# Kernel tuning notes

Hardware: AMD Instinct MI355X
Metric: run time of the kernel (lower is better)

## Reference

```python
import jax, jax.numpy as jnp
import numpy as np

EMBED_DIM = 1024
NUM_HEADS = 16
HEAD_DIM = EMBED_DIM // NUM_HEADS


def setup_inputs() -> dict:
    key = jax.random.key(0)
    kx, kw1, kb1, kw2, kb2 = jax.random.split(key, 5)
    D = EMBED_DIM
    # torch nn.Linear default init: U(-1/sqrt(in), 1/sqrt(in)); use scaled uniform
    lim = 1.0 / np.sqrt(D)
    return {
        "x": jax.random.normal(kx, (2, 2048, D), dtype=jnp.float32),
        "w_qkv": jax.random.uniform(kw1, (D, 3 * D), jnp.float32, -lim, lim),
        "b_qkv": jax.random.uniform(kb1, (3 * D,), jnp.float32, -lim, lim),
        "w_o": jax.random.uniform(kw2, (D, D), jnp.float32, -lim, lim),
        "b_o": jax.random.uniform(kb2, (D,), jnp.float32, -lim, lim),
    }


def reference(x, w_qkv, b_qkv, w_o, b_o):
    B, S, D = x.shape
    H, hd = NUM_HEADS, HEAD_DIM
    qkv = x @ w_qkv + b_qkv                       # [B,S,3D]
    qkv = qkv.reshape(B, S, H, 3, hd)             # per-head [q|k|v] blocks of size hd
    q = qkv[:, :, :, 0].transpose(0, 2, 1, 3)     # [B,H,S,hd]
    k = qkv[:, :, :, 1].transpose(0, 2, 1, 3)
    v = qkv[:, :, :, 2].transpose(0, 2, 1, 3)
    scale = hd ** -0.5
    scores = jnp.einsum('bhqd,bhkd->bhqk', q, k) * scale
    attn = jax.nn.softmax(scores, axis=-1)
    out = jnp.einsum('bhqk,bhkd->bhqd', attn, v)  # [B,H,S,hd]
    out = out.transpose(0, 2, 1, 3).reshape(B, S, D)
    return out @ w_o + b_o
```

## Files before the change

kernel.cpp:

```cpp
#include <hip/hip_runtime.h>

typedef __attribute__((ext_vector_type(8))) _Float16 half8;
typedef __attribute__((ext_vector_type(4))) _Float16 half4;
typedef __attribute__((ext_vector_type(4))) float f32x4;
typedef __attribute__((ext_vector_type(16))) float f32x16;
typedef __attribute__((ext_vector_type(4))) int i32x4;

typedef __attribute__((address_space(1))) void* gptr_t;
typedef __attribute__((address_space(3))) void* lptr_t;
#define GLL16(g, l) __builtin_amdgcn_global_load_lds((gptr_t)(g), (lptr_t)(l), 16, 0, 0)

__device__ __forceinline__ float fast_exp2(float x) {
  float r;
  asm volatile("v_exp_f32 %0, %1" : "=v"(r) : "v"(x));
  return r;
}


__global__ void cvt_x_kernel(const float* __restrict__ x, _Float16* __restrict__ xh) {
  size_t i = (size_t)blockIdx.x * blockDim.x + threadIdx.x;
  float4 v = *reinterpret_cast<const float4*>(x + i * 4);
  half4 o = { (_Float16)v.x, (_Float16)v.y, (_Float16)v.z, (_Float16)v.w };
  *reinterpret_cast<half4*>(xh + i * 4) = o;
}

__global__ void transpose_cvt_kernel(const float* __restrict__ w, _Float16* __restrict__ wt, int N) {
  int tid = blockIdx.x * blockDim.x + threadIdx.x;
  int n = tid % N, kc = tid / N;
  half8 o;
#pragma unroll
  for (int i = 0; i < 8; ++i) o[i] = (_Float16)w[(size_t)(kc * 8 + i) * N + n];
  *reinterpret_cast<half8*>(wt + (size_t)n * 1024 + kc * 8) = o;
}


template<int EPI>
__global__ __launch_bounds__(256, 2)
void gemm16(const _Float16* __restrict__ A, const _Float16* __restrict__ Bt,
            const float* __restrict__ bias,
            _Float16* __restrict__ qh, _Float16* __restrict__ kh,
            _Float16* __restrict__ vT, float* __restrict__ outf) {
  __shared__ __align__(16) _Float16 Ah[128 * 64];
  __shared__ __align__(16) _Float16 Bh[128 * 64];
  const int t = threadIdx.x;
  const int w = t >> 6, ln = t & 63, G = ln >> 4, c = ln & 15;
  const int m0 = blockIdx.y * 128, n0 = blockIdx.x * 128;
  const int wr = w >> 1, wc = w & 1;
  f32x4 acc[4][4] = {};
  for (int kt = 0; kt < 1024; kt += 64) {
#pragma unroll
    for (int i = 0; i < 4; ++i) {
      int ch = i * 256 + t;
      int row = ch >> 3, kc = ch & 7;
      int kk = kt + ((kc ^ (row & 7)) << 3);
      int ldsbase = (i * 256 + w * 64) * 8;
      GLL16(A + (size_t)(m0 + row) * 1024 + kk, Ah + ldsbase);
      GLL16(Bt + (size_t)(n0 + row) * 1024 + kk, Bh + ldsbase);
    }
    __syncthreads();
    half8 aF[2][4], bF[2][4];
#pragma unroll
    for (int ks = 0; ks < 2; ++ks)
#pragma unroll
      for (int i = 0; i < 4; ++i) {
        int ra = wr * 64 + i * 16 + c;
        aF[ks][i] = *reinterpret_cast<const half8*>(&Ah[ra * 64 + (((ks * 4 + G) ^ (ra & 7)) << 3)]);
        int rb = wc * 64 + i * 16 + c;
        bF[ks][i] = *reinterpret_cast<const half8*>(&Bh[rb * 64 + (((ks * 4 + G) ^ (rb & 7)) << 3)]);
      }
#pragma unroll
    for (int ks = 0; ks < 2; ++ks)
#pragma unroll
      for (int mi = 0; mi < 4; ++mi)
#pragma unroll
        for (int ni = 0; ni < 4; ++ni)
          acc[mi][ni] = __builtin_amdgcn_mfma_f32_16x16x32_f16(aF[ks][mi], bF[ks][ni], acc[mi][ni], 0, 0, 0);
    __syncthreads();
  }
  const int mbase = m0 + wr * 64, nbase = n0 + wc * 64;
  const int Gp = ((G & 1) << 1) | (G >> 1);
#pragma unroll
  for (int ni = 0; ni < 4; ++ni) {
    int n = nbase + ni * 16 + c;
    float bv = bias[n];
    if (EPI == 0) {
      int h = n / 192;
      int rem = n - h * 192;
      int tt = rem >> 6, d = rem & 63;
#pragma unroll
      for (int mi = 0; mi < 4; ++mi) {
        if (tt == 2) {
          int mb = mbase + mi * 16;
          int bb = mb >> 11, s0 = mb & 2047;
          size_t bh = (size_t)(bb * 16 + h);
          half4 o = { (_Float16)(acc[mi][ni][0] + bv), (_Float16)(acc[mi][ni][1] + bv),
                      (_Float16)(acc[mi][ni][2] + bv), (_Float16)(acc[mi][ni][3] + bv) };
          *reinterpret_cast<half4*>(&vT[(bh * 64 + d) * 2048 + s0 + 4 * Gp]) = o;
        } else {
#pragma unroll
          for (int r = 0; r < 4; ++r) {
            int m = mbase + mi * 16 + 4 * G + r;
            int bb = m >> 11, s = m & 2047;
            float val = acc[mi][ni][r] + bv;
            size_t bh = (size_t)(bb * 16 + h);
            if (tt == 0) qh[(bh * 2048 + s) * 64 + d] = (_Float16)(val * (0.125f * 1.44269504089f));
            else         kh[(bh * 2048 + s) * 64 + d] = (_Float16)val;
          }
        }
      }
    } else {
#pragma unroll
      for (int mi = 0; mi < 4; ++mi)
#pragma unroll
        for (int r = 0; r < 4; ++r) {
          int m = mbase + mi * 16 + 4 * G + r;
          outf[(size_t)m * 1024 + n] = acc[mi][ni][r] + bv;
        }
    }
  }
}


__global__ __launch_bounds__(256, 2)
void attn_kernel(const _Float16* __restrict__ qh, const _Float16* __restrict__ kh,
                 const _Float16* __restrict__ vT, _Float16* __restrict__ ao) {
  __shared__ __align__(16) _Float16 Kt[2][64 * 64];
  __shared__ __align__(16) _Float16 Vt[2][64 * 64];
  const int t = threadIdx.x;
  const int w = t >> 6, ln = t & 63, lo = ln & 31, hi = ln >> 5;
  const int bid = blockIdx.x;
  const int xcd = bid & 7, tt = bid >> 3;
  const int bh = xcd * 4 + (tt >> 4);
  const int qb = tt & 15;
  const int q0 = qb * 128 + w * 32;
  const _Float16* qp = qh + (size_t)bh * 2048 * 64;
  const _Float16* kp = kh + (size_t)bh * 2048 * 64;
  const _Float16* vp = vT + (size_t)bh * 64 * 2048;

  half8 qf[4];
#pragma unroll
  for (int sl = 0; sl < 4; ++sl)
    qf[sl] = *reinterpret_cast<const half8*>(qp + (size_t)(q0 + lo) * 64 + sl * 16 + hi * 8);

  f32x16 O0 = {}, O1 = {};
  float mrun = -INFINITY, lsum = 0.f;

  auto stage = [&](int b, int jt) {
#pragma unroll
    for (int i = 0; i < 2; ++i) {
      int ch = i * 256 + t;
      int row = ch >> 3, cc = ch & 7;
      int sw = ((cc ^ (row & 7)) << 3);
      int ldsbase = (i * 256 + w * 64) * 8;
      GLL16(kp + (size_t)(jt + row) * 64 + sw, &Kt[b][ldsbase]);
      GLL16(vp + (size_t)row * 2048 + jt + sw, &Vt[b][ldsbase]);
    }
  };

  stage(0, 0);
  __syncthreads();

  for (int it = 0; it < 32; ++it) {
    const int buf = it & 1;
    if (it < 31) stage(buf ^ 1, (it + 1) * 64);

    f32x16 st0 = {}, st1 = {};
    __builtin_amdgcn_s_setprio(1);
#pragma unroll
    for (int sl = 0; sl < 4; ++sl) {
      const int ch = sl * 2 + hi;
      half8 k0 = *reinterpret_cast<const half8*>(&Kt[buf][lo * 64 + ((ch ^ (lo & 7)) << 3)]);
      half8 k1 = *reinterpret_cast<const half8*>(&Kt[buf][(32 + lo) * 64 + ((ch ^ ((32 + lo) & 7)) << 3)]);
      st0 = __builtin_amdgcn_mfma_f32_32x32x16_f16(k0, qf[sl], st0, 0, 0, 0);
      st1 = __builtin_amdgcn_mfma_f32_32x32x16_f16(k1, qf[sl], st1, 0, 0, 0);
    }
    __builtin_amdgcn_s_setprio(0);

    float mx[8];
#pragma unroll
    for (int i = 0; i < 8; ++i) mx[i] = fmaxf(fmaxf(st0[i], st0[i + 8]), fmaxf(st1[i], st1[i + 8]));
#pragma unroll
    for (int i = 0; i < 4; ++i) mx[i] = fmaxf(mx[i], mx[i + 4]);
    float tm = fmaxf(fmaxf(mx[0], mx[1]), fmaxf(mx[2], mx[3]));
    tm = fmaxf(tm, __shfl_xor(tm, 32));
    if (!__all(tm <= mrun + 8.f)) {
      float mnew = fmaxf(mrun, tm);
      float corr = fast_exp2(mrun - mnew);
      lsum *= corr;
#pragma unroll
      for (int i = 0; i < 16; ++i) { O0[i] *= corr; O1[i] *= corr; }
      mrun = mnew;
    }
#pragma unroll
    for (int i = 0; i < 16; ++i) st0[i] = fast_exp2(st0[i] - mrun);
#pragma unroll
    for (int i = 0; i < 16; ++i) st1[i] = fast_exp2(st1[i] - mrun);
    float sm[8];
#pragma unroll
    for (int i = 0; i < 8; ++i) sm[i] = (st0[i] + st0[i + 8]) + (st1[i] + st1[i + 8]);
#pragma unroll
    for (int i = 0; i < 4; ++i) sm[i] += sm[i + 4];
    float ps = (sm[0] + sm[1]) + (sm[2] + sm[3]);
    ps += __shfl_xor(ps, 32);
    lsum += ps;

    unsigned pk[4][4];
#pragma unroll
    for (int kh2 = 0; kh2 < 2; ++kh2)
#pragma unroll
      for (int j = 0; j < 4; ++j) {
        pk[kh2][j]     = __builtin_bit_cast(unsigned, __builtin_amdgcn_cvt_pkrtz(st0[kh2 * 8 + 2 * j], st0[kh2 * 8 + 2 * j + 1]));
        pk[2 + kh2][j] = __builtin_bit_cast(unsigned, __builtin_amdgcn_cvt_pkrtz(st1[kh2 * 8 + 2 * j], st1[kh2 * 8 + 2 * j + 1]));
      }

    __builtin_amdgcn_s_setprio(1);
#pragma unroll
    for (int kb2 = 0; kb2 < 4; ++kb2) {
      i32x4 pi = { (int)pk[kb2][0], (int)pk[kb2][1], (int)pk[kb2][2], (int)pk[kb2][3] };
      half8 pf = __builtin_bit_cast(half8, pi);
      const int ch = kb2 * 2 + hi;
      half8 v0 = *reinterpret_cast<const half8*>(&Vt[buf][lo * 64 + ((ch ^ (lo & 7)) << 3)]);
      half8 v1 = *reinterpret_cast<const half8*>(&Vt[buf][(32 + lo) * 64 + ((ch ^ ((32 + lo) & 7)) << 3)]);
      O0 = __builtin_amdgcn_mfma_f32_32x32x16_f16(v0, pf, O0, 0, 0, 0);
      O1 = __builtin_amdgcn_mfma_f32_32x32x16_f16(v1, pf, O1, 0, 0, 0);
    }
    __builtin_amdgcn_s_setprio(0);
    __syncthreads();
  }

  float inv = 1.f / lsum;
  const int bb = bh >> 4, h = bh & 15;
  const size_t srow = (size_t)bb * 2048 + q0 + lo;
  _Float16* aob = ao + srow * 1024 + h * 64 + hi * 4;
#pragma unroll
  for (int rq = 0; rq < 4; ++rq) {
    half4 o0 = { (_Float16)(O0[4 * rq] * inv), (_Float16)(O0[4 * rq + 1] * inv),
                 (_Float16)(O0[4 * rq + 2] * inv), (_Float16)(O0[4 * rq + 3] * inv) };
    *reinterpret_cast<half4*>(aob + rq * 8) = o0;
    half4 o1 = { (_Float16)(O1[4 * rq] * inv), (_Float16)(O1[4 * rq + 1] * inv),
                 (_Float16)(O1[4 * rq + 2] * inv), (_Float16)(O1[4 * rq + 3] * inv) };
    *reinterpret_cast<half4*>(aob + 32 + rq * 8) = o1;
  }
}


extern "C" void kernel_launch(void* const* d_in, const int* in_sizes, int n_in,
                              void* d_out, int out_size, void* d_ws, size_t ws_size,
                              hipStream_t stream) {
  const float* x     = (const float*)d_in[0];
  const float* w_qkv = (const float*)d_in[1];
  const float* b_qkv = (const float*)d_in[2];
  const float* w_o   = (const float*)d_in[3];
  const float* b_o   = (const float*)d_in[4];
  float* out = (float*)d_out;
  char* ws = (char*)d_ws;
  _Float16* xh    = (_Float16*)(ws);
  _Float16* wqkvT = (_Float16*)(ws + ((size_t)8  << 20));
  _Float16* woT   = (_Float16*)(ws + ((size_t)14 << 20));
  _Float16* qh    = (_Float16*)(ws + ((size_t)16 << 20));
  _Float16* kh    = (_Float16*)(ws + ((size_t)24 << 20));
  _Float16* vT    = (_Float16*)(ws + ((size_t)32 << 20));
  _Float16* ao    = (_Float16*)(ws + ((size_t)40 << 20));

  cvt_x_kernel<<<4096, 256, 0, stream>>>(x, xh);
  transpose_cvt_kernel<<<1536, 256, 0, stream>>>(w_qkv, wqkvT, 3072);
  transpose_cvt_kernel<<<512, 256, 0, stream>>>(w_o, woT, 1024);
  gemm16<0><<<dim3(24, 32), 256, 0, stream>>>(xh, wqkvT, b_qkv, qh, kh, vT, nullptr);
  attn_kernel<<<512, 256, 0, stream>>>(qh, kh, vT, ao);
  gemm16<1><<<dim3(8, 32), 256, 0, stream>>>(ao, woT, b_o, nullptr, nullptr, nullptr, out);
}
```

Measured before the change: 133.7 us.

## Software-pipeline attention: overlap next QK^T with current PV, 64 rows per wave

The attention kernel now runs 2 waves per block, each handling 64 query rows as two 32-row fragments, so every K/V fragment read from LDS is reused for two MFMAs. The loop is software-pipelined: the QK^T for tile it+1 is issued alongside the PV for tile it, with a triple-buffered V and double-buffered K staged two tiles ahead. This aims to hide softmax and exp latency behind MFMA work and cut LDS traffic per FLOP. In exchange it doubles the accumulator register state and reduces waves per block, which may lower occupancy or cause spills.

After: 190.4 us. +42.4%, slower.

```diff
diff --git a/kernel.cpp b/kernel.cpp
--- a/kernel.cpp
+++ b/kernel.cpp
@@ -121,125 +121,163 @@
 }
 
 
-__global__ __launch_bounds__(256, 2)
+__global__ __launch_bounds__(128, 2)
 void attn_kernel(const _Float16* __restrict__ qh, const _Float16* __restrict__ kh,
                  const _Float16* __restrict__ vT, _Float16* __restrict__ ao) {
   __shared__ __align__(16) _Float16 Kt[2][64 * 64];
-  __shared__ __align__(16) _Float16 Vt[2][64 * 64];
+  __shared__ __align__(16) _Float16 Vt[3][64 * 64];
   const int t = threadIdx.x;
   const int w = t >> 6, ln = t & 63, lo = ln & 31, hi = ln >> 5;
   const int bid = blockIdx.x;
   const int xcd = bid & 7, tt = bid >> 3;
   const int bh = xcd * 4 + (tt >> 4);
   const int qb = tt & 15;
-  const int q0 = qb * 128 + w * 32;
+  const int q0 = qb * 128 + w * 64;
   const _Float16* qp = qh + (size_t)bh * 2048 * 64;
   const _Float16* kp = kh + (size_t)bh * 2048 * 64;
   const _Float16* vp = vT + (size_t)bh * 64 * 2048;
 
-  half8 qf[4];
-#pragma unroll
-  for (int sl = 0; sl < 4; ++sl)
-    qf[sl] = *reinterpret_cast<const half8*>(qp + (size_t)(q0 + lo) * 64 + sl * 16 + hi * 8);
-
-  f32x16 O0 = {}, O1 = {};
-  float mrun = -INFINITY, lsum = 0.f;
-
-  auto stage = [&](int b, int jt) {
-#pragma unroll
-    for (int i = 0; i < 2; ++i) {
-      int ch = i * 256 + t;
+  half8 qf[2][4];
+#pragma unroll
+  for (int f = 0; f < 2; ++f)
+#pragma unroll
+    for (int sl = 0; sl < 4; ++sl)
+      qf[f][sl] = *reinterpret_cast<const half8*>(qp + (size_t)(q0 + f * 32 + lo) * 64 + sl * 16 + hi * 8);
+
+  f32x16 O00 = {}, O01 = {}, O10 = {}, O11 = {};
+  float mrun0 = -INFINITY, mrun1 = -INFINITY, lsum0 = 0.f, lsum1 = 0.f;
+  unsigned pk[2][4][4];
+
+  auto stage = [&](int kb, int vb3, int jt) {
+#pragma unroll
+    for (int i = 0; i < 4; ++i) {
+      int ch = i * 128 + t;
       int row = ch >> 3, cc = ch & 7;
       int sw = ((cc ^ (row & 7)) << 3);
-      int ldsbase = (i * 256 + w * 64) * 8;
-      GLL16(kp + (size_t)(jt + row) * 64 + sw, &Kt[b][ldsbase]);
-      GLL16(vp + (size_t)row * 2048 + jt + sw, &Vt[b][ldsbase]);
+      int ldsbase = (i * 128 + w * 64) * 8;
+      GLL16(kp + (size_t)(jt + row) * 64 + sw, &Kt[kb][ldsbase]);
+      GLL16(vp + (size_t)row * 2048 + jt + sw, &Vt[vb3][ldsbase]);
     }
   };
 
-  stage(0, 0);
-  __syncthreads();
-
-  for (int it = 0; it < 32; ++it) {
-    const int buf = it & 1;
-    if (it < 31) stage(buf ^ 1, (it + 1) * 64);
-
-    f32x16 st0 = {}, st1 = {};
-    __builtin_amdgcn_s_setprio(1);
+  auto qkt = [&](int kb, f32x16 st[2][2]) {
 #pragma unroll
     for (int sl = 0; sl < 4; ++sl) {
       const int ch = sl * 2 + hi;
-      half8 k0 = *reinterpret_cast<const half8*>(&Kt[buf][lo * 64 + ((ch ^ (lo & 7)) << 3)]);
-      half8 k1 = *reinterpret_cast<const half8*>(&Kt[buf][(32 + lo) * 64 + ((ch ^ ((32 + lo) & 7)) << 3)]);
-      st0 = __builtin_amdgcn_mfma_f32_32x32x16_f16(k0, qf[sl], st0, 0, 0, 0);
-      st1 = __builtin_amdgcn_mfma_f32_32x32x16_f16(k1, qf[sl], st1, 0, 0, 0);
-    }
-    __builtin_amdgcn_s_setprio(0);
-
+      const int sw = (ch ^ (lo & 7)) << 3;
+      half8 k0 = *reinterpret_cast<const half8*>(&Kt[kb][lo * 64 + sw]);
+      st[0][0] = __builtin_amdgcn_mfma_f32_32x32x16_f16(k0, qf[0][sl], st[0][0], 0, 0, 0);
+      st[1][0] = __builtin_amdgcn_mfma_f32_32x32x16_f16(k0, qf[1][sl], st[1][0], 0, 0, 0);
+      half8 k1 = *reinterpret_cast<const half8*>(&Kt[kb][(32 + lo) * 64 + sw]);
+      st[0][1] = __builtin_amdgcn_mfma_f32_32x32x16_f16(k1, qf[0][sl], st[0][1], 0, 0, 0);
+      st[1][1] = __builtin_amdgcn_mfma_f32_32x32x16_f16(k1, qf[1][sl], st[1][1], 0, 0, 0);
+    }
+  };
+
+  auto pv = [&](int vb3) {
+#pragma unroll
+    for (int kb2 = 0; kb2 < 4; ++kb2) {
+      i32x4 pi0 = { (int)pk[0][kb2][0], (int)pk[0][kb2][1], (int)pk[0][kb2][2], (int)pk[0][kb2][3] };
+      i32x4 pi1 = { (int)pk[1][kb2][0], (int)pk[1][kb2][1], (int)pk[1][kb2][2], (int)pk[1][kb2][3] };
+      half8 pf0 = __builtin_bit_cast(half8, pi0);
+      half8 pf1 = __builtin_bit_cast(half8, pi1);
+      const int ch = kb2 * 2 + hi;
+      const int sw = (ch ^ (lo & 7)) << 3;
+      half8 v0 = *reinterpret_cast<const half8*>(&Vt[vb3][lo * 64 + sw]);
+      O00 = __builtin_amdgcn_mfma_f32_32x32x16_f16(v0, pf0, O00, 0, 0, 0);
+      O10 = __builtin_amdgcn_mfma_f32_32x32x16_f16(v0, pf1, O10, 0, 0, 0);
+      half8 v1 = *reinterpret_cast<const half8*>(&Vt[vb3][(32 + lo) * 64 + sw]);
+      O01 = __builtin_amdgcn_mfma_f32_32x32x16_f16(v1, pf0, O01, 0, 0, 0);
+      O11 = __builtin_amdgcn_mfma_f32_32x32x16_f16(v1, pf1, O11, 0, 0, 0);
+    }
+  };
+
+  auto softmax_pack = [&](f32x16& s0, f32x16& s1, float& mr, float& ls,
+                          f32x16& Oa, f32x16& Ob, unsigned pkf[4][4]) {
     float mx[8];
 #pragma unroll
-    for (int i = 0; i < 8; ++i) mx[i] = fmaxf(fmaxf(st0[i], st0[i + 8]), fmaxf(st1[i], st1[i + 8]));
+    for (int i = 0; i < 8; ++i) mx[i] = fmaxf(fmaxf(s0[i], s0[i + 8]), fmaxf(s1[i], s1[i + 8]));
 #pragma unroll
     for (int i = 0; i < 4; ++i) mx[i] = fmaxf(mx[i], mx[i + 4]);
     float tm = fmaxf(fmaxf(mx[0], mx[1]), fmaxf(mx[2], mx[3]));
     tm = fmaxf(tm, __shfl_xor(tm, 32));
-    if (!__all(tm <= mrun + 8.f)) {
-      float mnew = fmaxf(mrun, tm);
-      float corr = fast_exp2(mrun - mnew);
-      lsum *= corr;
-#pragma unroll
-      for (int i = 0; i < 16; ++i) { O0[i] *= corr; O1[i] *= corr; }
-      mrun = mnew;
-    }
-#pragma unroll
-    for (int i = 0; i < 16; ++i) st0[i] = fast_exp2(st0[i] - mrun);
-#pragma unroll
-    for (int i = 0; i < 16; ++i) st1[i] = fast_exp2(st1[i] - mrun);
+    if (!__all(tm <= mr + 8.f)) {
+      float mnew = fmaxf(mr, tm);
+      float corr = fast_exp2(mr - mnew);
+      ls *= corr;
+#pragma unroll
+      for (int i = 0; i < 16; ++i) { Oa[i] *= corr; Ob[i] *= corr; }
+      mr = mnew;
+    }
+#pragma unroll
+    for (int i = 0; i < 16; ++i) s0[i] = fast_exp2(s0[i] - mr);
+#pragma unroll
+    for (int i = 0; i < 16; ++i) s1[i] = fast_exp2(s1[i] - mr);
     float sm[8];
 #pragma unroll
-    for (int i = 0; i < 8; ++i) sm[i] = (st0[i] + st0[i + 8]) + (st1[i] + st1[i + 8]);
+    for (int i = 0; i < 8; ++i) sm[i] = (s0[i] + s0[i + 8]) + (s1[i] + s1[i + 8]);
 #pragma unroll
     for (int i = 0; i < 4; ++i) sm[i] += sm[i + 4];
     float ps = (sm[0] + sm[1]) + (sm[2] + sm[3]);
     ps += __shfl_xor(ps, 32);
-    lsum += ps;
-
-    unsigned pk[4][4];
+    ls += ps;
 #pragma unroll
     for (int kh2 = 0; kh2 < 2; ++kh2)
 #pragma unroll
       for (int j = 0; j < 4; ++j) {
-        pk[kh2][j]     = __builtin_bit_cast(unsigned, __builtin_amdgcn_cvt_pkrtz(st0[kh2 * 8 + 2 * j], st0[kh2 * 8 + 2 * j + 1]));
-        pk[2 + kh2][j] = __builtin_bit_cast(unsigned, __builtin_amdgcn_cvt_pkrtz(st1[kh2 * 8 + 2 * j], st1[kh2 * 8 + 2 * j + 1]));
+        pkf[kh2][j]     = __builtin_bit_cast(unsigned, __builtin_amdgcn_cvt_pkrtz(s0[kh2 * 8 + 2 * j], s0[kh2 * 8 + 2 * j + 1]));
+        pkf[2 + kh2][j] = __builtin_bit_cast(unsigned, __builtin_amdgcn_cvt_pkrtz(s1[kh2 * 8 + 2 * j], s1[kh2 * 8 + 2 * j + 1]));
       }
-
+  };
+
+  stage(0, 0, 0);
+  stage(1, 1, 64);
+  __syncthreads();
+  {
+    f32x16 st[2][2] = {};
+    qkt(0, st);
+    softmax_pack(st[0][0], st[0][1], mrun0, lsum0, O00, O01, pk[0]);
+    softmax_pack(st[1][0], st[1][1], mrun1, lsum1, O10, O11, pk[1]);
+  }
+  __syncthreads();
+
+  int vb = 0;
+  for (int it = 0; it < 31; ++it) {
+    if (it < 30) {
+      int vb2 = vb + 2; if (vb2 >= 3) vb2 -= 3;
+      stage(it & 1, vb2, (it + 2) * 64);
+    }
+    f32x16 st[2][2] = {};
     __builtin_amdgcn_s_setprio(1);
-#pragma unroll
-    for (int kb2 = 0; kb2 < 4; ++kb2) {
-      i32x4 pi = { (int)pk[kb2][0], (int)pk[kb2][1], (int)pk[kb2][2], (int)pk[kb2][3] };
-      half8 pf = __builtin_bit_cast(half8, pi);
-      const int ch = kb2 * 2 + hi;
-      half8 v0 = *reinterpret_cast<const half8*>(&Vt[buf][lo * 64 + ((ch ^ (lo & 7)) << 3)]);
-      half8 v1 = *reinterpret_cast<const half8*>(&Vt[buf][(32 + lo) * 64 + ((ch ^ ((32 + lo) & 7)) << 3)]);
-      O0 = __builtin_amdgcn_mfma_f32_32x32x16_f16(v0, pf, O0, 0, 0, 0);
-      O1 = __builtin_amdgcn_mfma_f32_32x32x16_f16(v1, pf, O1, 0, 0, 0);
-    }
+    qkt((it + 1) & 1, st);
+    pv(vb);
     __builtin_amdgcn_s_setprio(0);
+    softmax_pack(st[0][0], st[0][1], mrun0, lsum0, O00, O01, pk[0]);
+    softmax_pack(st[1][0], st[1][1], mrun1, lsum1, O10, O11, pk[1]);
     __syncthreads();
-  }
-
-  float inv = 1.f / lsum;
-  const int bb = bh >> 4, h = bh & 15;
-  const size_t srow = (size_t)bb * 2048 + q0 + lo;
-  _Float16* aob = ao + srow * 1024 + h * 64 + hi * 4;
+    ++vb; if (vb == 3) vb = 0;
+  }
+  pv(vb);
+
+  const int bb = bh >> 4, hd_i = bh & 15;
+  float inv0 = 1.f / lsum0, inv1 = 1.f / lsum1;
+  const size_t srow0 = (size_t)bb * 2048 + q0 + lo;
+  _Float16* aob0 = ao + srow0 * 1024 + hd_i * 64 + hi * 4;
+  _Float16* aob1 = aob0 + (size_t)32 * 1024;
 #pragma unroll
   for (int rq = 0; rq < 4; ++rq) {
-    half4 o0 = { (_Float16)(O0[4 * rq] * inv), (_Float16)(O0[4 * rq + 1] * inv),
-                 (_Float16)(O0[4 * rq + 2] * inv), (_Float16)(O0[4 * rq + 3] * inv) };
-    *reinterpret_cast<half4*>(aob + rq * 8) = o0;
-    half4 o1 = { (_Float16)(O1[4 * rq] * inv), (_Float16)(O1[4 * rq + 1] * inv),
-                 (_Float16)(O1[4 * rq + 2] * inv), (_Float16)(O1[4 * rq + 3] * inv) };
-    *reinterpret_cast<half4*>(aob + 32 + rq * 8) = o1;
+    half4 a0 = { (_Float16)(O00[4 * rq] * inv0), (_Float16)(O00[4 * rq + 1] * inv0),
+                 (_Float16)(O00[4 * rq + 2] * inv0), (_Float16)(O00[4 * rq + 3] * inv0) };
+    *reinterpret_cast<half4*>(aob0 + rq * 8) = a0;
+    half4 a1 = { (_Float16)(O01[4 * rq] * inv0), (_Float16)(O01[4 * rq + 1] * inv0),
+                 (_Float16)(O01[4 * rq + 2] * inv0), (_Float16)(O01[4 * rq + 3] * inv0) };
+    *reinterpret_cast<half4*>(aob0 + 32 + rq * 8) = a1;
+    half4 b0 = { (_Float16)(O10[4 * rq] * inv1), (_Float16)(O10[4 * rq + 1] * inv1),
+                 (_Float16)(O10[4 * rq + 2] * inv1), (_Float16)(O10[4 * rq + 3] * inv1) };
+    *reinterpret_cast<half4*>(aob1 + rq * 8) = b0;
+    half4 b1 = { (_Float16)(O11[4 * rq] * inv1), (_Float16)(O11[4 * rq + 1] * inv1),
+                 (_Float16)(O11[4 * rq + 2] * inv1), (_Float16)(O11[4 * rq + 3] * inv1) };
+    *reinterpret_cast<half4*>(aob1 + 32 + rq * 8) = b1;
   }
 }
 
@@ -266,6 +304,6 @@
   transpose_cvt_kernel<<<1536, 256, 0, stream>>>(w_qkv, wqkvT, 3072);
   transpose_cvt_kernel<<<512, 256, 0, stream>>>(w_o, woT, 1024);
   gemm16<0><<<dim3(24, 32), 256, 0, stream>>>(xh, wqkvT, b_qkv, qh, kh, vT, nullptr);
-  attn_kernel<<<512, 256, 0, stream>>>(qh, kh, vT, ao);
+  attn_kernel<<<512, 128, 0, stream>>>(qh, kh, vT, ao);
   gemm16<1><<<dim3(8, 32), 256, 0, stream>>>(ao, woT, b_o, nullptr, nullptr, nullptr, out);
 }
```
